# Kernel tuning notes

Measured on AMD Instinct MI355X. Metric: run time of the kernel, lower is better.

Reference implementation:

```python
import jax, jax.numpy as jnp
import numpy as np

EPS = 1e-6
NEG_SLOPE = 0.2

B, C_IN, N, K = 4, 64, 40960, 16
C_OUT = 64


def setup_inputs() -> dict:
    key = jax.random.key(0)
    k1, k2, k3 = jax.random.split(key, 3)
    feature = jax.random.normal(k1, (B, C_IN, N, 1), dtype=jnp.float32)
    neigh_idx = jax.random.randint(k2, (B, N, K), 0, N, dtype=jnp.int64)
    # 1x1 conv kernel [C_out, C_in] (kaiming-like scale), no bias since bn=True
    W = jax.random.normal(k3, (C_OUT, C_IN), dtype=jnp.float32) * np.float32(np.sqrt(2.0 / C_IN))
    gamma = jnp.ones((C_OUT,), dtype=jnp.float32)
    beta = jnp.zeros((C_OUT,), dtype=jnp.float32)
    return {"feature": feature, "W": W, "gamma": gamma, "beta": beta, "neigh_idx": neigh_idx}


def _gather_neighbour(pc, neigh_idx):
    # pc: [B, C, N]; neigh_idx: [B, N, K] -> [B, C, N, K]
    return jax.vmap(lambda p, idx: p[:, idx])(pc, neigh_idx)


def reference(feature, W, gamma, beta, neigh_idx):
    pc = feature[..., 0]                       # [B, C, N]
    f_neigh = _gather_neighbour(pc, neigh_idx) # [B, C, N, K]
    x = jnp.concatenate([feature, f_neigh], axis=-1)  # [B, C, N, K+1]
    # 1x1 conv (no bias)
    y = jnp.einsum('oc,bcnk->bonk', W, x)      # [B, C_out, N, K+1]
    # BatchNorm2d (training mode: batch stats over B,N,K+1), eps=1e-6
    mean = jnp.mean(y, axis=(0, 2, 3), keepdims=True)
    var = jnp.mean(jnp.square(y - mean), axis=(0, 2, 3), keepdims=True)
    yn = (y - mean) * jax.lax.rsqrt(var + EPS)
    yn = yn * gamma[None, :, None, None] + beta[None, :, None, None]
    # LeakyReLU(0.2)
    act = jnp.where(yn >= 0, yn, NEG_SLOPE * yn)
    # sum over neighbor axis, keepdim
    return jnp.sum(act, axis=-1, keepdims=True)  # [B, C_out, N, 1]
```

## Files before the change

### kernel.cpp

```cpp
#include <hip/hip_runtime.h>
#include <hip/hip_fp16.h>

typedef _Float16 h2 __attribute__((ext_vector_type(2)));

#define BB 4
#define CIN 64
#define COUT 64
#define NN 40960
#define KK 16
#define GBLK (BB * NN / 256)
#define FPAD 264
#define WPAD 68
#define HP 32
#define HR 2
#define HBINS (NN / HR)
#define HWORDS (HBINS / 2)

__global__ __launch_bounds__(256) void k_hist(const int* __restrict__ idx,
                                              unsigned int* __restrict__ hist) {
    __shared__ unsigned int bins[HWORDS];
    const int tid = threadIdx.x;
    const int b = blockIdx.x >> 6;
    const int p = (blockIdx.x >> 1) & (HP - 1);
    const int r = blockIdx.x & (HR - 1);
    const int lo = r * HBINS;

#pragma unroll
    for (int i = 0; i < HWORDS / 256; ++i) bins[i * 256 + tid] = 0u;
    __syncthreads();

    const int SHARE = NN * KK / HP;
    const int4* src = (const int4*)(idx + (size_t)b * NN * KK + (size_t)p * SHARE);
#pragma unroll 4
    for (int i = 0; i < SHARE / 4 / 256; ++i) {
        int4 v = src[i * 256 + tid];
        unsigned a0 = (unsigned)(v.x - lo), a1 = (unsigned)(v.y - lo);
        unsigned a2 = (unsigned)(v.z - lo), a3 = (unsigned)(v.w - lo);
        if (a0 < HBINS) atomicAdd(&bins[a0 >> 1], 1u << ((a0 & 1) * 16));
        if (a1 < HBINS) atomicAdd(&bins[a1 >> 1], 1u << ((a1 & 1) * 16));
        if (a2 < HBINS) atomicAdd(&bins[a2 >> 1], 1u << ((a2 & 1) * 16));
        if (a3 < HBINS) atomicAdd(&bins[a3 >> 1], 1u << ((a3 & 1) * 16));
    }
    __syncthreads();
    unsigned int* dst = hist + (size_t)blockIdx.x * HWORDS;
#pragma unroll
    for (int i = 0; i < HWORDS / 256; ++i) dst[i * 256 + tid] = bins[i * 256 + tid];
}

__global__ __launch_bounds__(256) void k_gemm(const float* __restrict__ feat,
                                              const float* __restrict__ W,
                                              const unsigned int* __restrict__ hist,
                                              __half* __restrict__ g,
                                              float* __restrict__ partials) {
    __shared__ float Wt_s[64 * WPAD];
    __shared__ float feat_s[16 * FPAD];
    __shared__ float w_s[256];

    const int tid = threadIdx.x;
    const int b   = blockIdx.x / (NN / 256);
    const int n0  = (blockIdx.x % (NN / 256)) * 256;

    {
        const int n  = n0 + tid;
        const int r  = n / HBINS;
        const int ml = n - r * HBINS;
        const int w  = ml >> 1;
        const int sh = (ml & 1) * 16;
        unsigned s = 1u;
#pragma unroll
        for (int p = 0; p < HP; ++p)
            s += (hist[(size_t)((b * HP + p) * HR + r) * HWORDS + w] >> sh) & 0xffffu;
        w_s[tid] = (float)s;
    }

#pragma unroll
    for (int it = 0; it < 16; ++it) {
        int c = tid & 63;
        int o = it * 4 + (tid >> 6);
        Wt_s[c * WPAD + o] = W[o * 64 + c];
    }

    const int to = tid & 7;
    const int tn = tid >> 3;

    float acc[8][8];
#pragma unroll
    for (int i = 0; i < 8; ++i)
#pragma unroll
        for (int j = 0; j < 8; ++j) acc[i][j] = 0.f;

    const float* fb = feat + (size_t)b * CIN * NN + n0;

    for (int cc0 = 0; cc0 < 64; cc0 += 16) {
        __syncthreads();
        {
            int row = tid >> 4;
            int col = (tid & 15) * 4;
            const float* src = fb + (size_t)(cc0 + row) * NN + col;
#pragma unroll
            for (int q = 0; q < 4; ++q) {
                float4 v = *(const float4*)(src + q * 64);
                *(float4*)&feat_s[row * FPAD + col + q * 64] = v;
            }
        }
        __syncthreads();

#pragma unroll
        for (int cc = 0; cc < 16; ++cc) {
            int c = cc0 + cc;
            float4 w0 = *(const float4*)&Wt_s[c * WPAD + to * 8];
            float4 w1 = *(const float4*)&Wt_s[c * WPAD + to * 8 + 4];
            float4 f0 = *(const float4*)&feat_s[cc * FPAD + tn * 8];
            float4 f1 = *(const float4*)&feat_s[cc * FPAD + tn * 8 + 4];
            float wv[8] = {w0.x, w0.y, w0.z, w0.w, w1.x, w1.y, w1.z, w1.w};
            float fv[8] = {f0.x, f0.y, f0.z, f0.w, f1.x, f1.y, f1.z, f1.w};
#pragma unroll
            for (int i = 0; i < 8; ++i)
#pragma unroll
                for (int j = 0; j < 8; ++j)
                    acc[i][j] = fmaf(wv[i], fv[j], acc[i][j]);
        }
    }

    __half* gb = g + ((size_t)b * NN + n0) * 64;
#pragma unroll
    for (int j = 0; j < 8; ++j) {
        int n = tn * 8 + j;
        union { uint4 u; h2 h[4]; } P;
#pragma unroll
        for (int h = 0; h < 4; ++h) {
            h2 t;
            t.x = (_Float16)acc[2 * h][j];
            t.y = (_Float16)acc[2 * h + 1][j];
            P.h[h] = t;
        }
        *(uint4*)&gb[(size_t)n * 64 + to * 8] = P.u;
    }

    float wgt[8];
#pragma unroll
    for (int j = 0; j < 8; ++j) wgt[j] = w_s[tn * 8 + j];
    float s1[8], s2[8];
#pragma unroll
    for (int i = 0; i < 8; ++i) { s1[i] = 0.f; s2[i] = 0.f; }
#pragma unroll
    for (int j = 0; j < 8; ++j)
#pragma unroll
        for (int i = 0; i < 8; ++i) {
            float wv = wgt[j] * acc[i][j];
            s1[i] += wv;
            s2[i] += wv * acc[i][j];
        }

    __syncthreads();
    float* red = feat_s;
#pragma unroll
    for (int i = 0; i < 8; ++i) {
        int o = to * 8 + i;
        red[o * 33 + tn]        = s1[i];
        red[2112 + o * 33 + tn] = s2[i];
    }
    __syncthreads();
    if (tid < 128) {
        int arr = tid >> 6, o = tid & 63;
        const float* base = red + arr * 2112 + o * 33;
        float s = 0.f;
#pragma unroll
        for (int t = 0; t < 32; ++t) s += base[t];
        partials[blockIdx.x * 128 + arr * 64 + o] = s;
    }
}

__global__ __launch_bounds__(1024) void k_finalize(const float* __restrict__ partials,
                                                   const float* __restrict__ gamma,
                                                   const float* __restrict__ beta,
                                                   _Float16* __restrict__ params_h) {
    const int i = threadIdx.x & 127;
    const int r = threadIdx.x >> 7;
    double a0 = 0, a1 = 0, a2 = 0, a3 = 0;
    for (int base = r; base < GBLK; base += 32) {
        a0 += (double)partials[(base)      * 128 + i];
        a1 += (double)partials[(base + 8)  * 128 + i];
        a2 += (double)partials[(base + 16) * 128 + i];
        a3 += (double)partials[(base + 24) * 128 + i];
    }
    __shared__ double red[8][128];
    red[r][i] = (a0 + a1) + (a2 + a3);
    __syncthreads();
    if (threadIdx.x < 64) {
        const int o = threadIdx.x;
        double s1 = 0.0, s2 = 0.0;
#pragma unroll
        for (int rr = 0; rr < 8; ++rr) { s1 += red[rr][o]; s2 += red[rr][64 + o]; }
        const double TOT = (double)BB * NN * (KK + 1);
        double mean = s1 / TOT;
        double var  = s2 / TOT - mean * mean;
        double inv  = 1.0 / sqrt(var + 1e-6);
        float scale = (float)inv * gamma[o];
        float shift = beta[o] - (float)mean * scale;
        params_h[o]      = (_Float16)scale;
        params_h[64 + o] = (_Float16)shift;
    }
}

__global__ __launch_bounds__(256) void k_final(const __half* __restrict__ g,
                                               const int* __restrict__ idx,
                                               const _Float16* __restrict__ params_h,
                                               float* __restrict__ out) {
    const int tid  = threadIdx.x;
    const int lane = tid & 63;
    const int wave = tid >> 6;
    const int b     = (blockIdx.x & 7) >> 1;
    const int chunk = ((blockIdx.x >> 3) << 1) | (blockIdx.x & 1);
    const int n0    = chunk * 64;

    __shared__ int   idx_s[64 * 17];
    __shared__ float tile[64 * 65];

    {
        const int4* src = (const int4*)(idx + ((size_t)b * NN + n0) * KK);
        int4 v = src[tid];
        int row = tid >> 2, col = (tid & 3) * 4;
        idx_s[row * 17 + col + 0] = v.x;
        idx_s[row * 17 + col + 1] = v.y;
        idx_s[row * 17 + col + 2] = v.z;
        idx_s[row * 17 + col + 3] = v.w;
    }

    const int r  = lane >> 3;
    const int q8 = (lane & 7) * 8;
    h2 sc2[4], sh2[4];
#pragma unroll
    for (int h = 0; h < 4; ++h) {
        h2 a, s;
        a.x = params_h[q8 + 2 * h];     a.y = params_h[q8 + 2 * h + 1];
        s.x = params_h[64 + q8 + 2 * h]; s.y = params_h[64 + q8 + 2 * h + 1];
        sc2[h] = a; sh2[h] = s;
    }
    __syncthreads();

    const __half* gb = g + (size_t)b * NN * 64;

#pragma unroll
    for (int rr = 0; rr < 2; ++rr) {
        const int nl = wave * 16 + rr * 8 + r;
        h2 acc[4];
#pragma unroll
        for (int h = 0; h < 4; ++h) acc[h] = (h2)(_Float16)0;

#pragma unroll
        for (int k = -1; k < KK; ++k) {
            int m = (k < 0) ? (n0 + nl) : idx_s[nl * 17 + k];
            union { uint4 u; h2 h[4]; } U;
            U.u = *(const uint4*)(gb + (size_t)m * 64 + q8);
#pragma unroll
            for (int h = 0; h < 4; ++h) {
                h2 t = U.h[h] * sc2[h] + sh2[h];
                acc[h] += __builtin_elementwise_max(t, t * (_Float16)0.2f);
            }
        }
        float* tr = &tile[nl * 65 + q8];
#pragma unroll
        for (int h = 0; h < 4; ++h) {
            tr[2 * h]     = (float)acc[h].x;
            tr[2 * h + 1] = (float)acc[h].y;
        }
    }
    __syncthreads();
    const int j   = tid & 63;
    const int sub = tid >> 6;
#pragma unroll
    for (int ob = 0; ob < 16; ++ob) {
        int o = ob * 4 + sub;
        out[(size_t)(b * 64 + o) * NN + n0 + j] = tile[j * 65 + o];
    }
}

extern "C" void kernel_launch(void* const* d_in, const int* in_sizes, int n_in,
                              void* d_out, int out_size, void* d_ws, size_t ws_size,
                              hipStream_t stream) {
    const float* feat  = (const float*)d_in[0];
    const float* W     = (const float*)d_in[1];
    const float* gamma = (const float*)d_in[2];
    const float* beta  = (const float*)d_in[3];
    const int*   idx   = (const int*)d_in[4];
    float* out = (float*)d_out;

    char* ws = (char*)d_ws;
    __half* g = (__half*)ws;
    size_t off = (size_t)BB * NN * 64 * sizeof(__half);
    unsigned int* hist = (unsigned int*)(ws + off);
    off += (size_t)BB * HP * HR * HWORDS * sizeof(unsigned int);
    float* partials = (float*)(ws + off);
    off += (size_t)GBLK * 128 * sizeof(float);
    _Float16* params_h = (_Float16*)(ws + off);

    k_hist<<<BB * HP * HR, 256, 0, stream>>>(idx, hist);
    k_gemm<<<GBLK, 256, 0, stream>>>(feat, W, hist, g, partials);
    k_finalize<<<1, 1024, 0, stream>>>(partials, gamma, beta, params_h);
    k_final<<<(BB * NN) / 64, 256, 0, stream>>>(g, idx, params_h, out);
}
```

Measured before the change: 158.3 us.

## Split gathered features into channel halves and pack histogram as byte counters

The fp16 projected features are stored as two separate 32-channel arrays, and each final-stage block gathers only one half for 256 points. This shrinks the per-neighbour gather footprint and should improve cache locality of the random gather. The histogram now uses 8-bit packed counters over the full index range in a single pass, which removes the range-split blocks, and the GEMM reads those counts directly as bytes. The output transpose writes float4 stores, at the cost of larger shared tiles and a risk of 8-bit counter overflow if a point receives more than 255 references within one partition.

```diff
diff --git a/kernel.cpp b/kernel.cpp
--- a/kernel.cpp
+++ b/kernel.cpp
@@ -12,18 +12,15 @@
 #define FPAD 264
 #define WPAD 68
 #define HP 32
-#define HR 2
-#define HBINS (NN / HR)
-#define HWORDS (HBINS / 2)
+#define HWORDS (NN / 4)
+#define TP 37
 
 __global__ __launch_bounds__(256) void k_hist(const int* __restrict__ idx,
                                               unsigned int* __restrict__ hist) {
     __shared__ unsigned int bins[HWORDS];
     const int tid = threadIdx.x;
-    const int b = blockIdx.x >> 6;
-    const int p = (blockIdx.x >> 1) & (HP - 1);
-    const int r = blockIdx.x & (HR - 1);
-    const int lo = r * HBINS;
+    const int b = blockIdx.x >> 5;
+    const int p = blockIdx.x & (HP - 1);
 
 #pragma unroll
     for (int i = 0; i < HWORDS / 256; ++i) bins[i * 256 + tid] = 0u;
@@ -34,12 +31,10 @@
 #pragma unroll 4
     for (int i = 0; i < SHARE / 4 / 256; ++i) {
         int4 v = src[i * 256 + tid];
-        unsigned a0 = (unsigned)(v.x - lo), a1 = (unsigned)(v.y - lo);
-        unsigned a2 = (unsigned)(v.z - lo), a3 = (unsigned)(v.w - lo);
-        if (a0 < HBINS) atomicAdd(&bins[a0 >> 1], 1u << ((a0 & 1) * 16));
-        if (a1 < HBINS) atomicAdd(&bins[a1 >> 1], 1u << ((a1 & 1) * 16));
-        if (a2 < HBINS) atomicAdd(&bins[a2 >> 1], 1u << ((a2 & 1) * 16));
-        if (a3 < HBINS) atomicAdd(&bins[a3 >> 1], 1u << ((a3 & 1) * 16));
+        atomicAdd(&bins[(unsigned)v.x >> 2], 1u << (((unsigned)v.x & 3) * 8));
+        atomicAdd(&bins[(unsigned)v.y >> 2], 1u << (((unsigned)v.y & 3) * 8));
+        atomicAdd(&bins[(unsigned)v.z >> 2], 1u << (((unsigned)v.z & 3) * 8));
+        atomicAdd(&bins[(unsigned)v.w >> 2], 1u << (((unsigned)v.w & 3) * 8));
     }
     __syncthreads();
     unsigned int* dst = hist + (size_t)blockIdx.x * HWORDS;
@@ -49,8 +44,9 @@
 
 __global__ __launch_bounds__(256) void k_gemm(const float* __restrict__ feat,
                                               const float* __restrict__ W,
-                                              const unsigned int* __restrict__ hist,
-                                              __half* __restrict__ g,
+                                              const unsigned char* __restrict__ hist,
+                                              __half* __restrict__ g_lo,
+                                              __half* __restrict__ g_hi,
                                               float* __restrict__ partials) {
     __shared__ float Wt_s[64 * WPAD];
     __shared__ float feat_s[16 * FPAD];
@@ -61,15 +57,11 @@
     const int n0  = (blockIdx.x % (NN / 256)) * 256;
 
     {
-        const int n  = n0 + tid;
-        const int r  = n / HBINS;
-        const int ml = n - r * HBINS;
-        const int w  = ml >> 1;
-        const int sh = (ml & 1) * 16;
+        const int n = n0 + tid;
         unsigned s = 1u;
 #pragma unroll
         for (int p = 0; p < HP; ++p)
-            s += (hist[(size_t)((b * HP + p) * HR + r) * HWORDS + w] >> sh) & 0xffffu;
+            s += hist[(size_t)(b * HP + p) * NN + n];
         w_s[tid] = (float)s;
     }
 
@@ -122,7 +114,8 @@
         }
     }
 
-    __half* gb = g + ((size_t)b * NN + n0) * 64;
+    __half* glo_b = g_lo + ((size_t)b * NN + n0) * 32;
+    __half* ghi_b = g_hi + ((size_t)b * NN + n0) * 32;
 #pragma unroll
     for (int j = 0; j < 8; ++j) {
         int n = tn * 8 + j;
@@ -134,7 +127,9 @@
             t.y = (_Float16)acc[2 * h + 1][j];
             P.h[h] = t;
         }
-        *(uint4*)&gb[(size_t)n * 64 + to * 8] = P.u;
+        __half* dst = (to < 4) ? (glo_b + (size_t)n * 32 + to * 8)
+                               : (ghi_b + (size_t)n * 32 + (to - 4) * 8);
+        *(uint4*)dst = P.u;
     }
 
     float wgt[8];
@@ -203,76 +198,86 @@
     }
 }
 
-__global__ __launch_bounds__(256) void k_final(const __half* __restrict__ g,
+__global__ __launch_bounds__(256) void k_final(const __half* __restrict__ g_lo,
+                                               const __half* __restrict__ g_hi,
                                                const int* __restrict__ idx,
                                                const _Float16* __restrict__ params_h,
                                                float* __restrict__ out) {
     const int tid  = threadIdx.x;
     const int lane = tid & 63;
     const int wave = tid >> 6;
-    const int b     = (blockIdx.x & 7) >> 1;
-    const int chunk = ((blockIdx.x >> 3) << 1) | (blockIdx.x & 1);
-    const int n0    = chunk * 64;
-
-    __shared__ int   idx_s[64 * 17];
-    __shared__ float tile[64 * 65];
+    const int p     = blockIdx.x & 7;
+    const int chunk = blockIdx.x >> 3;
+    const int b     = p >> 1;
+    const int h     = p & 1;
+    const int n0    = chunk * 256;
+
+    __shared__ int   idx_s[256 * 17];
+    __shared__ float tile[256 * TP];
 
     {
         const int4* src = (const int4*)(idx + ((size_t)b * NN + n0) * KK);
-        int4 v = src[tid];
-        int row = tid >> 2, col = (tid & 3) * 4;
-        idx_s[row * 17 + col + 0] = v.x;
-        idx_s[row * 17 + col + 1] = v.y;
-        idx_s[row * 17 + col + 2] = v.z;
-        idx_s[row * 17 + col + 3] = v.w;
-    }
-
-    const int r  = lane >> 3;
-    const int q8 = (lane & 7) * 8;
+#pragma unroll
+        for (int i = 0; i < 4; ++i) {
+            int e = i * 256 + tid;
+            int4 v = src[e];
+            int pt = e >> 2, k4 = (e & 3) * 4;
+            idx_s[pt * 17 + k4 + 0] = v.x;
+            idx_s[pt * 17 + k4 + 1] = v.y;
+            idx_s[pt * 17 + k4 + 2] = v.z;
+            idx_s[pt * 17 + k4 + 3] = v.w;
+        }
+    }
+
+    const int q = (lane & 3) * 8;
     h2 sc2[4], sh2[4];
 #pragma unroll
-    for (int h = 0; h < 4; ++h) {
+    for (int hh = 0; hh < 4; ++hh) {
         h2 a, s;
-        a.x = params_h[q8 + 2 * h];     a.y = params_h[q8 + 2 * h + 1];
-        s.x = params_h[64 + q8 + 2 * h]; s.y = params_h[64 + q8 + 2 * h + 1];
-        sc2[h] = a; sh2[h] = s;
-    }
-    __syncthreads();
-
-    const __half* gb = g + (size_t)b * NN * 64;
-
-#pragma unroll
-    for (int rr = 0; rr < 2; ++rr) {
-        const int nl = wave * 16 + rr * 8 + r;
+        a.x = params_h[h * 32 + q + 2 * hh];      a.y = params_h[h * 32 + q + 2 * hh + 1];
+        s.x = params_h[64 + h * 32 + q + 2 * hh]; s.y = params_h[64 + h * 32 + q + 2 * hh + 1];
+        sc2[hh] = a; sh2[hh] = s;
+    }
+    __syncthreads();
+
+    const __half* gb = (h ? g_hi : g_lo) + (size_t)b * NN * 32;
+
+#pragma unroll
+    for (int it = 0; it < 4; ++it) {
+        const int pt = wave * 64 + it * 16 + (lane >> 2);
         h2 acc[4];
 #pragma unroll
-        for (int h = 0; h < 4; ++h) acc[h] = (h2)(_Float16)0;
+        for (int hh = 0; hh < 4; ++hh) acc[hh] = (h2)(_Float16)0;
 
 #pragma unroll
         for (int k = -1; k < KK; ++k) {
-            int m = (k < 0) ? (n0 + nl) : idx_s[nl * 17 + k];
+            int m = (k < 0) ? (n0 + pt) : idx_s[pt * 17 + k];
             union { uint4 u; h2 h[4]; } U;
-            U.u = *(const uint4*)(gb + (size_t)m * 64 + q8);
-#pragma unroll
-            for (int h = 0; h < 4; ++h) {
-                h2 t = U.h[h] * sc2[h] + sh2[h];
-                acc[h] += __builtin_elementwise_max(t, t * (_Float16)0.2f);
+            U.u = *(const uint4*)(gb + (size_t)m * 32 + q);
+#pragma unroll
+            for (int hh = 0; hh < 4; ++hh) {
+                h2 t = U.h[hh] * sc2[hh] + sh2[hh];
+                acc[hh] += __builtin_elementwise_max(t, t * (_Float16)0.2f);
             }
         }
-        float* tr = &tile[nl * 65 + q8];
-#pragma unroll
-        for (int h = 0; h < 4; ++h) {
-            tr[2 * h]     = (float)acc[h].x;
-            tr[2 * h + 1] = (float)acc[h].y;
-        }
-    }
-    __syncthreads();
-    const int j   = tid & 63;
-    const int sub = tid >> 6;
-#pragma unroll
-    for (int ob = 0; ob < 16; ++ob) {
-        int o = ob * 4 + sub;
-        out[(size_t)(b * 64 + o) * NN + n0 + j] = tile[j * 65 + o];
+        float* tr = &tile[pt * TP + q];
+#pragma unroll
+        for (int hh = 0; hh < 4; ++hh) {
+            tr[2 * hh]     = (float)acc[hh].x;
+            tr[2 * hh + 1] = (float)acc[hh].y;
+        }
+    }
+    __syncthreads();
+
+    const int oo   = tid >> 3;
+    const int nsub = tid & 7;
+    float* ob = out + ((size_t)(b * 64 + h * 32 + oo)) * NN + n0;
+#pragma unroll
+    for (int pass = 0; pass < 8; ++pass) {
+        int nl = pass * 32 + nsub * 4;
+        float4 v = make_float4(tile[(nl + 0) * TP + oo], tile[(nl + 1) * TP + oo],
+                               tile[(nl + 2) * TP + oo], tile[(nl + 3) * TP + oo]);
+        *(float4*)&ob[nl] = v;
     }
 }
 
@@ -287,16 +292,18 @@
     float* out = (float*)d_out;
 
     char* ws = (char*)d_ws;
-    __half* g = (__half*)ws;
-    size_t off = (size_t)BB * NN * 64 * sizeof(__half);
-    unsigned int* hist = (unsigned int*)(ws + off);
-    off += (size_t)BB * HP * HR * HWORDS * sizeof(unsigned int);
+    __half* g_lo = (__half*)ws;
+    size_t off = (size_t)BB * NN * 32 * sizeof(__half);
+    __half* g_hi = (__half*)(ws + off);
+    off += (size_t)BB * NN * 32 * sizeof(__half);
+    unsigned char* hist = (unsigned char*)(ws + off);
+    off += (size_t)BB * HP * NN;
     float* partials = (float*)(ws + off);
     off += (size_t)GBLK * 128 * sizeof(float);
     _Float16* params_h = (_Float16*)(ws + off);
 
-    k_hist<<<BB * HP * HR, 256, 0, stream>>>(idx, hist);
-    k_gemm<<<GBLK, 256, 0, stream>>>(feat, W, hist, g, partials);
+    k_hist<<<BB * HP, 256, 0, stream>>>(idx, (unsigned int*)hist);
+    k_gemm<<<GBLK, 256, 0, stream>>>(feat, W, hist, g_lo, g_hi, partials);
     k_finalize<<<1, 1024, 0, stream>>>(partials, gamma, beta, params_h);
-    k_final<<<(BB * NN) / 64, 256, 0, stream>>>(g, idx, params_h, out);
-}
+    k_final<<<8 * (NN / 256), 256, 0, stream>>>(g_lo, g_hi, idx, params_h, out);
+}
```

After: 159.9 us. No clear change (+1.0%).
